# Performance work log

Hardware: AMD Instinct MI355X
Metric: run time of the kernel (lower is better)

## Reference

```python
import jax, jax.numpy as jnp
import numpy as np

NVFP4_VALUES = jnp.array([0.0, 0.5, 1.0, 1.5, 2.0, 3.0, 4.0, 6.0], dtype=jnp.float32)
NVFP4_MAX = 6.0


def quantize_to_nvfp4(t):
    """Fake-quantize to NVFP4 (e2m1) via nearest codebook magnitude.
    Returns (quantized_tensor, inv_scale) matching the torch reference."""
    amax = jnp.maximum(jnp.max(jnp.abs(t)), 1e-12)
    scale = NVFP4_MAX / amax                      # scalar
    scaled = jnp.clip(t.astype(jnp.float32) * scale, -NVFP4_MAX, NVFP4_MAX)
    signs = jnp.sign(scaled)
    # distance to each of the 8 e2m1 magnitudes -> nearest index
    dist = jnp.abs(jnp.abs(scaled)[..., None] - NVFP4_VALUES)  # (..., 8)
    idx = jnp.argmin(dist, axis=-1)
    quantized = signs * NVFP4_VALUES[idx]
    return quantized, 1.0 / scale


def setup_inputs() -> dict:
    key = jax.random.key(0)
    kx, kw = jax.random.split(key)
    x = jax.random.normal(kx, (512, 4096), dtype=jnp.float32)          # batch=512 (in SUPPORTED_BATCH_SIZES -> no padding)
    # kaiming-uniform-ish init for weight [out_features, in_features]
    bound = float(np.sqrt(6.0 / 4096.0))
    weight = jax.random.uniform(kw, (4096, 4096), dtype=jnp.float32,
                                minval=-bound, maxval=bound)
    return {"x": x, "weight": weight}


def reference(x, weight):
    # batch==512 is an exact supported size, so pad/unpad is identity.
    x_q, x_inv_scale = quantize_to_nvfp4(x)
    w_q, w_inv_scale = quantize_to_nvfp4(weight)
    # out[b,o] = sum_i (x_q*x_s)[b,i] * (w_q*w_s)[o,i]
    out = jnp.einsum('bi,oi->bo', x_q * x_inv_scale, w_q * w_inv_scale)
    return out.astype(x.dtype)
```

## Files before the change

### kernel.cpp

```cpp
#include <hip/hip_runtime.h>

#define M_DIM 512
#define N_DIM 4096
#define K_DIM 4096

typedef __attribute__((ext_vector_type(4))) float f32x4;
typedef __attribute__((ext_vector_type(8))) int i32x8;
typedef __attribute__((ext_vector_type(4))) int i32x4;

#define PART_X_OFF 0
#define PART_X_N   256
#define PART_W_OFF 256
#define PART_W_N   1024
#define AMAX_OFF   1280
#define XQ_BYTE_OFF 8192
#define WQ_BYTE_OFF (XQ_BYTE_OFF + M_DIM * K_DIM)

__global__ __launch_bounds__(256) void amax_kernel(
    const float4* __restrict__ x4, const float4* __restrict__ w4,
    float* __restrict__ ws_f) {
    const int b = blockIdx.x;
    float m = 0.0f;
    if (b < PART_X_N) {
        const int n4 = M_DIM * K_DIM / 4, stride = PART_X_N * 256;
        for (int i = b * 256 + threadIdx.x; i < n4; i += stride) {
            float4 a = x4[i];
            m = fmaxf(m, fmaxf(fmaxf(fabsf(a.x), fabsf(a.y)),
                               fmaxf(fabsf(a.z), fabsf(a.w))));
        }
    } else {
        const int n4 = N_DIM * K_DIM / 4, stride = PART_W_N * 256;
        for (int i = (b - PART_X_N) * 256 + threadIdx.x; i < n4; i += stride) {
            float4 a = w4[i];
            m = fmaxf(m, fmaxf(fmaxf(fabsf(a.x), fabsf(a.y)),
                               fmaxf(fabsf(a.z), fabsf(a.w))));
        }
    }
    for (int off = 32; off > 0; off >>= 1)
        m = fmaxf(m, __shfl_down(m, off, 64));
    __shared__ float sm[4];
    if ((threadIdx.x & 63) == 0) sm[threadIdx.x >> 6] = m;
    __syncthreads();
    if (threadIdx.x == 0) {
        m = fmaxf(fmaxf(sm[0], sm[1]), fmaxf(sm[2], sm[3]));
        ws_f[(b < PART_X_N) ? (PART_X_OFF + b) : (PART_W_OFF + b - PART_X_N)] = m;
    }
}

__device__ __forceinline__ unsigned int q1(float x, float s) {
    float a = fabsf(x) * s;
    unsigned int b;
    if      (a <= 0.25f) b = 0x00u;
    else if (a <= 0.75f) b = 0x30u;
    else if (a <= 1.25f) b = 0x38u;
    else if (a <= 1.75f) b = 0x3Cu;
    else if (a <= 2.5f)  b = 0x40u;
    else if (a <= 3.5f)  b = 0x44u;
    else if (a <= 5.0f)  b = 0x48u;
    else                 b = 0x4Cu;
    return b | ((__float_as_uint(x) >> 24) & 0x80u);
}
__device__ __forceinline__ unsigned int qpack4(float4 v, float s) {
    return q1(v.x, s) | (q1(v.y, s) << 8) | (q1(v.z, s) << 16) | (q1(v.w, s) << 24);
}

__global__ __launch_bounds__(256) void quant_kernel(
    const float4* __restrict__ x4, const float4* __restrict__ w4,
    float* __restrict__ ws_f, unsigned char* __restrict__ ws_b) {
    const int b = blockIdx.x, t = threadIdx.x;
    const bool is_x = b < 512;
    float m = 0.0f;
    if (is_x) {
        m = ws_f[PART_X_OFF + t];
    } else {
        for (int i = t; i < PART_W_N; i += 256)
            m = fmaxf(m, ws_f[PART_W_OFF + i]);
    }
    for (int off = 32; off > 0; off >>= 1)
        m = fmaxf(m, __shfl_down(m, off, 64));
    __shared__ float sm[4];
    if ((t & 63) == 0) sm[t >> 6] = m;
    __syncthreads();
    m = fmaxf(fmaxf(sm[0], sm[1]), fmaxf(sm[2], sm[3]));
    float amax = fmaxf(m, 1e-12f);
    float s = 6.0f / amax;
    if (t == 0 && b == 0)   ws_f[AMAX_OFF + 0] = amax;
    if (t == 0 && b == 512) ws_f[AMAX_OFF + 1] = amax;

    const float4* src = is_x ? x4 : w4;
    unsigned char* dstb = ws_b + (is_x ? XQ_BYTE_OFF : WQ_BYTE_OFF);
    const int idx16 = (is_x ? b : b - 512) * 256 + t;
    const float4* p = src + (size_t)idx16 * 4;
    uint4 o;
    o.x = qpack4(p[0], s);
    o.y = qpack4(p[1], s);
    o.z = qpack4(p[2], s);
    o.w = qpack4(p[3], s);
    ((uint4*)dstb)[idx16] = o;
}

__device__ __forceinline__ void async_copy16(const void* g, void* l) {
    __builtin_amdgcn_global_load_lds(
        (const __attribute__((address_space(1))) unsigned int*)g,
        (__attribute__((address_space(3))) unsigned int*)l, 16, 0, 0);
}

__device__ __forceinline__ i32x8 frag_load(const unsigned char* rowbase,
                                           int mask, int g0) {
    const i32x4 lo = *(const i32x4*)(rowbase + ((g0 ^ mask) * 16));
    const i32x4 hi = *(const i32x4*)(rowbase + (((g0 + 1) ^ mask) * 16));
    return __builtin_shufflevector(lo, hi, 0, 1, 2, 3, 4, 5, 6, 7);
}

__global__ __launch_bounds__(256, 2) void gemm_kernel(
    const unsigned char* __restrict__ A, const unsigned char* __restrict__ B,
    float* __restrict__ C, const float* __restrict__ amax2) {
    __shared__ __align__(16) unsigned char As[64 * 512];
    __shared__ __align__(16) unsigned char Bs[64 * 512];

    const int bid  = blockIdx.x;
    const int bm   = (bid >> 6) * 64;
    const int bn   = ((bid & 7) * 8 + ((bid >> 3) & 7)) * 64;
    const int tid  = threadIdx.x;
    const int lane = tid & 63;
    const int wave = tid >> 6;
    const int wm   = (wave >> 1) * 32;
    const int wn   = (wave & 1) * 32;
    const int t15  = lane & 15;
    const int quad = lane >> 4;

    const float cs = (1.0f / (6.0f / fmaxf(amax2[0], 1e-12f))) *
                     (1.0f / (6.0f / fmaxf(amax2[1], 1e-12f)));

    const unsigned char* agp[8];
    const unsigned char* bgp[8];
#pragma unroll
    for (int j = 0; j < 8; j++) {
        const int c = j * 256 + tid;
        const int row = c >> 5, pcol = c & 31;
        const int gk = pcol ^ (row & 31);
        agp[j] = A + (size_t)(bm + row) * K_DIM + gk * 16;
        bgp[j] = B + (size_t)(bn + row) * K_DIM + gk * 16;
    }

    f32x4 acc[2][2] = {};
    const unsigned char* A0 = As + (size_t)(wm + t15) * 512;
    const unsigned char* A1 = A0 + 16 * 512;
    const unsigned char* B0 = Bs + (size_t)(wn + t15) * 512;
    const unsigned char* B1 = B0 + 16 * 512;
    const int mk0 = t15, mk1 = t15 + 16;

    for (int ko = 0; ko < K_DIM; ko += 512) {
#pragma unroll
        for (int j = 0; j < 8; j++) {
            async_copy16(agp[j] + ko, As + (j * 256 + tid) * 16);
            async_copy16(bgp[j] + ko, Bs + (j * 256 + tid) * 16);
        }
        __syncthreads();

#pragma unroll
        for (int s = 0; s < 4; s++) {
            const int g0 = s * 8 + (quad << 1);
            const i32x8 af0 = frag_load(A0, mk0, g0);
            const i32x8 af1 = frag_load(A1, mk1, g0);
            const i32x8 bf0 = frag_load(B0, mk0, g0);
            const i32x8 bf1 = frag_load(B1, mk1, g0);
            acc[0][0] = __builtin_amdgcn_mfma_scale_f32_16x16x128_f8f6f4(
                af0, bf0, acc[0][0], 0, 0, 0, 0x7F7F7F7F, 0, 0x7F7F7F7F);
            acc[0][1] = __builtin_amdgcn_mfma_scale_f32_16x16x128_f8f6f4(
                af0, bf1, acc[0][1], 0, 0, 0, 0x7F7F7F7F, 0, 0x7F7F7F7F);
            acc[1][0] = __builtin_amdgcn_mfma_scale_f32_16x16x128_f8f6f4(
                af1, bf0, acc[1][0], 0, 0, 0, 0x7F7F7F7F, 0, 0x7F7F7F7F);
            acc[1][1] = __builtin_amdgcn_mfma_scale_f32_16x16x128_f8f6f4(
                af1, bf1, acc[1][1], 0, 0, 0, 0x7F7F7F7F, 0, 0x7F7F7F7F);
        }
        __syncthreads();
    }

#pragma unroll
    for (int i = 0; i < 2; i++)
#pragma unroll
        for (int j = 0; j < 2; j++) {
            const int m0 = bm + wm + i * 16 + quad * 4;
            const int n0 = bn + wn + j * 16 + t15;
#pragma unroll
            for (int r = 0; r < 4; r++)
                C[(size_t)(m0 + r) * N_DIM + n0] = acc[i][j][r] * cs;
        }
}

extern "C" void kernel_launch(void* const* d_in, const int* in_sizes, int n_in,
                              void* d_out, int out_size, void* d_ws, size_t ws_size,
                              hipStream_t stream) {
    const float* x = (const float*)d_in[0];
    const float* w = (const float*)d_in[1];
    float* out = (float*)d_out;

    float* ws_f = (float*)d_ws;
    unsigned char* ws_b = (unsigned char*)d_ws;
    const unsigned char* xq = ws_b + XQ_BYTE_OFF;
    const unsigned char* wq = ws_b + WQ_BYTE_OFF;

    amax_kernel<<<PART_X_N + PART_W_N, 256, 0, stream>>>(
        (const float4*)x, (const float4*)w, ws_f);
    quant_kernel<<<512 + 4096, 256, 0, stream>>>(
        (const float4*)x, (const float4*)w, ws_f, ws_b);
    gemm_kernel<<<(M_DIM / 64) * (N_DIM / 64), 256, 0, stream>>>(
        xq, wq, out, ws_f + AMAX_OFF);
}
```

Baseline: 134.4 us.

## Fuse amax, quantize and GEMM into one cooperative kernel with grid syncs

Replaces the three separate launches (amax reduction, quantization, GEMM) with one cooperative kernel of 512 blocks that uses grid.sync between phases. Each block computes partial amax for x and w, then after a grid barrier reduces the partials, quantizes its slice, and after another barrier runs the same MFMA GEMM tile. The aim is to remove launch overhead and inter-kernel gaps. The cost is that the memory-bound amax and quant phases now run on only 512 blocks with fixed unrolled loops, which may lower bandwidth utilisation, plus two grid-wide barriers. The old three-kernel path is kept as a fallback if the cooperative launch fails.

Result: slower. 263.4 us (+96.0%).

```diff
diff --git a/kernel.cpp b/kernel.cpp
--- a/kernel.cpp
+++ b/kernel.cpp
@@ -1,4 +1,7 @@
 #include <hip/hip_runtime.h>
+#include <hip/hip_cooperative_groups.h>
+
+namespace cg = cooperative_groups;
 
 #define M_DIM 512
 #define N_DIM 4096
@@ -8,6 +11,8 @@
 typedef __attribute__((ext_vector_type(8))) int i32x8;
 typedef __attribute__((ext_vector_type(4))) int i32x4;
 
+#define F_PART_X   0
+#define F_PART_W   512
 #define PART_X_OFF 0
 #define PART_X_N   256
 #define PART_W_OFF 256
@@ -15,37 +20,6 @@
 #define AMAX_OFF   1280
 #define XQ_BYTE_OFF 8192
 #define WQ_BYTE_OFF (XQ_BYTE_OFF + M_DIM * K_DIM)
-
-__global__ __launch_bounds__(256) void amax_kernel(
-    const float4* __restrict__ x4, const float4* __restrict__ w4,
-    float* __restrict__ ws_f) {
-    const int b = blockIdx.x;
-    float m = 0.0f;
-    if (b < PART_X_N) {
-        const int n4 = M_DIM * K_DIM / 4, stride = PART_X_N * 256;
-        for (int i = b * 256 + threadIdx.x; i < n4; i += stride) {
-            float4 a = x4[i];
-            m = fmaxf(m, fmaxf(fmaxf(fabsf(a.x), fabsf(a.y)),
-                               fmaxf(fabsf(a.z), fabsf(a.w))));
-        }
-    } else {
-        const int n4 = N_DIM * K_DIM / 4, stride = PART_W_N * 256;
-        for (int i = (b - PART_X_N) * 256 + threadIdx.x; i < n4; i += stride) {
-            float4 a = w4[i];
-            m = fmaxf(m, fmaxf(fmaxf(fabsf(a.x), fabsf(a.y)),
-                               fmaxf(fabsf(a.z), fabsf(a.w))));
-        }
-    }
-    for (int off = 32; off > 0; off >>= 1)
-        m = fmaxf(m, __shfl_down(m, off, 64));
-    __shared__ float sm[4];
-    if ((threadIdx.x & 63) == 0) sm[threadIdx.x >> 6] = m;
-    __syncthreads();
-    if (threadIdx.x == 0) {
-        m = fmaxf(fmaxf(sm[0], sm[1]), fmaxf(sm[2], sm[3]));
-        ws_f[(b < PART_X_N) ? (PART_X_OFF + b) : (PART_W_OFF + b - PART_X_N)] = m;
-    }
-}
 
 __device__ __forceinline__ unsigned int q1(float x, float s) {
     float a = fabsf(x) * s;
@@ -64,41 +38,6 @@
     return q1(v.x, s) | (q1(v.y, s) << 8) | (q1(v.z, s) << 16) | (q1(v.w, s) << 24);
 }
 
-__global__ __launch_bounds__(256) void quant_kernel(
-    const float4* __restrict__ x4, const float4* __restrict__ w4,
-    float* __restrict__ ws_f, unsigned char* __restrict__ ws_b) {
-    const int b = blockIdx.x, t = threadIdx.x;
-    const bool is_x = b < 512;
-    float m = 0.0f;
-    if (is_x) {
-        m = ws_f[PART_X_OFF + t];
-    } else {
-        for (int i = t; i < PART_W_N; i += 256)
-            m = fmaxf(m, ws_f[PART_W_OFF + i]);
-    }
-    for (int off = 32; off > 0; off >>= 1)
-        m = fmaxf(m, __shfl_down(m, off, 64));
-    __shared__ float sm[4];
-    if ((t & 63) == 0) sm[t >> 6] = m;
-    __syncthreads();
-    m = fmaxf(fmaxf(sm[0], sm[1]), fmaxf(sm[2], sm[3]));
-    float amax = fmaxf(m, 1e-12f);
-    float s = 6.0f / amax;
-    if (t == 0 && b == 0)   ws_f[AMAX_OFF + 0] = amax;
-    if (t == 0 && b == 512) ws_f[AMAX_OFF + 1] = amax;
-
-    const float4* src = is_x ? x4 : w4;
-    unsigned char* dstb = ws_b + (is_x ? XQ_BYTE_OFF : WQ_BYTE_OFF);
-    const int idx16 = (is_x ? b : b - 512) * 256 + t;
-    const float4* p = src + (size_t)idx16 * 4;
-    uint4 o;
-    o.x = qpack4(p[0], s);
-    o.y = qpack4(p[1], s);
-    o.z = qpack4(p[2], s);
-    o.w = qpack4(p[3], s);
-    ((uint4*)dstb)[idx16] = o;
-}
-
 __device__ __forceinline__ void async_copy16(const void* g, void* l) {
     __builtin_amdgcn_global_load_lds(
         (const __attribute__((address_space(1))) unsigned int*)g,
@@ -112,25 +51,93 @@
     return __builtin_shufflevector(lo, hi, 0, 1, 2, 3, 4, 5, 6, 7);
 }
 
-__global__ __launch_bounds__(256, 2) void gemm_kernel(
-    const unsigned char* __restrict__ A, const unsigned char* __restrict__ B,
-    float* __restrict__ C, const float* __restrict__ amax2) {
+__global__ __launch_bounds__(256, 2) void fused_kernel(
+    const float4* __restrict__ x4, const float4* __restrict__ w4,
+    float* __restrict__ C, float* __restrict__ ws_f,
+    unsigned char* __restrict__ ws_b) {
     __shared__ __align__(16) unsigned char As[64 * 512];
     __shared__ __align__(16) unsigned char Bs[64 * 512];
 
-    const int bid  = blockIdx.x;
-    const int bm   = (bid >> 6) * 64;
-    const int bn   = ((bid & 7) * 8 + ((bid >> 3) & 7)) * 64;
-    const int tid  = threadIdx.x;
+    const int b = blockIdx.x;
+    const int tid = threadIdx.x;
+    cg::grid_group grid = cg::this_grid();
+    float* sred = (float*)As;
+
+    {
+        float mx = 0.0f, mw = 0.0f;
+        const int base = b * 256 + tid, stride = 512 * 256;
+#pragma unroll
+        for (int j = 0; j < 4; j++) {
+            float4 a = x4[base + j * stride];
+            mx = fmaxf(mx, fmaxf(fmaxf(fabsf(a.x), fabsf(a.y)),
+                                 fmaxf(fabsf(a.z), fabsf(a.w))));
+        }
+#pragma unroll
+        for (int j = 0; j < 32; j++) {
+            float4 a = w4[base + j * stride];
+            mw = fmaxf(mw, fmaxf(fmaxf(fabsf(a.x), fabsf(a.y)),
+                                 fmaxf(fabsf(a.z), fabsf(a.w))));
+        }
+        for (int off = 32; off > 0; off >>= 1) {
+            mx = fmaxf(mx, __shfl_down(mx, off, 64));
+            mw = fmaxf(mw, __shfl_down(mw, off, 64));
+        }
+        if ((tid & 63) == 0) { sred[tid >> 6] = mx; sred[4 + (tid >> 6)] = mw; }
+        __syncthreads();
+        if (tid == 0) {
+            ws_f[F_PART_X + b] = fmaxf(fmaxf(sred[0], sred[1]),
+                                       fmaxf(sred[2], sred[3]));
+            ws_f[F_PART_W + b] = fmaxf(fmaxf(sred[4], sred[5]),
+                                       fmaxf(sred[6], sred[7]));
+        }
+    }
+    grid.sync();
+
+    float ax, aw;
+    {
+        float mx = fmaxf(ws_f[F_PART_X + tid], ws_f[F_PART_X + 256 + tid]);
+        float mw = fmaxf(ws_f[F_PART_W + tid], ws_f[F_PART_W + 256 + tid]);
+        for (int off = 32; off > 0; off >>= 1) {
+            mx = fmaxf(mx, __shfl_down(mx, off, 64));
+            mw = fmaxf(mw, __shfl_down(mw, off, 64));
+        }
+        if ((tid & 63) == 0) { sred[tid >> 6] = mx; sred[4 + (tid >> 6)] = mw; }
+        __syncthreads();
+        ax = fmaxf(fmaxf(fmaxf(sred[0], sred[1]), fmaxf(sred[2], sred[3])), 1e-12f);
+        aw = fmaxf(fmaxf(fmaxf(sred[4], sred[5]), fmaxf(sred[6], sred[7])), 1e-12f);
+        const float sx = 6.0f / ax, sw = 6.0f / aw;
+
+        {
+            const int idx16 = b * 256 + tid;
+            const float4* p = x4 + (size_t)idx16 * 4;
+            uint4 o;
+            o.x = qpack4(p[0], sx); o.y = qpack4(p[1], sx);
+            o.z = qpack4(p[2], sx); o.w = qpack4(p[3], sx);
+            ((uint4*)(ws_b + XQ_BYTE_OFF))[idx16] = o;
+        }
+#pragma unroll
+        for (int j = 0; j < 8; j++) {
+            const int idx16 = b * 2048 + j * 256 + tid;
+            const float4* p = w4 + (size_t)idx16 * 4;
+            uint4 o;
+            o.x = qpack4(p[0], sw); o.y = qpack4(p[1], sw);
+            o.z = qpack4(p[2], sw); o.w = qpack4(p[3], sw);
+            ((uint4*)(ws_b + WQ_BYTE_OFF))[idx16] = o;
+        }
+    }
+    const float cs = (1.0f / (6.0f / ax)) * (1.0f / (6.0f / aw));
+    grid.sync();
+
+    const unsigned char* A = ws_b + XQ_BYTE_OFF;
+    const unsigned char* B = ws_b + WQ_BYTE_OFF;
+    const int bm   = (b >> 6) * 64;
+    const int bn   = ((b & 7) * 8 + ((b >> 3) & 7)) * 64;
     const int lane = tid & 63;
     const int wave = tid >> 6;
     const int wm   = (wave >> 1) * 32;
     const int wn   = (wave & 1) * 32;
     const int t15  = lane & 15;
     const int quad = lane >> 4;
-
-    const float cs = (1.0f / (6.0f / fmaxf(amax2[0], 1e-12f))) *
-                     (1.0f / (6.0f / fmaxf(amax2[1], 1e-12f)));
 
     const unsigned char* agp[8];
     const unsigned char* bgp[8];
@@ -189,22 +196,166 @@
         }
 }
 
+__global__ __launch_bounds__(256) void amax_kernel(
+    const float4* __restrict__ x4, const float4* __restrict__ w4,
+    float* __restrict__ ws_f) {
+    const int b = blockIdx.x;
+    float m = 0.0f;
+    if (b < PART_X_N) {
+        const int n4 = M_DIM * K_DIM / 4, stride = PART_X_N * 256;
+        for (int i = b * 256 + threadIdx.x; i < n4; i += stride) {
+            float4 a = x4[i];
+            m = fmaxf(m, fmaxf(fmaxf(fabsf(a.x), fabsf(a.y)),
+                               fmaxf(fabsf(a.z), fabsf(a.w))));
+        }
+    } else {
+        const int n4 = N_DIM * K_DIM / 4, stride = PART_W_N * 256;
+        for (int i = (b - PART_X_N) * 256 + threadIdx.x; i < n4; i += stride) {
+            float4 a = w4[i];
+            m = fmaxf(m, fmaxf(fmaxf(fabsf(a.x), fabsf(a.y)),
+                               fmaxf(fabsf(a.z), fabsf(a.w))));
+        }
+    }
+    for (int off = 32; off > 0; off >>= 1)
+        m = fmaxf(m, __shfl_down(m, off, 64));
+    __shared__ float sm[4];
+    if ((threadIdx.x & 63) == 0) sm[threadIdx.x >> 6] = m;
+    __syncthreads();
+    if (threadIdx.x == 0) {
+        m = fmaxf(fmaxf(sm[0], sm[1]), fmaxf(sm[2], sm[3]));
+        ws_f[(b < PART_X_N) ? (PART_X_OFF + b) : (PART_W_OFF + b - PART_X_N)] = m;
+    }
+}
+
+__global__ __launch_bounds__(256) void quant_kernel(
+    const float4* __restrict__ x4, const float4* __restrict__ w4,
+    float* __restrict__ ws_f, unsigned char* __restrict__ ws_b) {
+    const int b = blockIdx.x, t = threadIdx.x;
+    const bool is_x = b < 512;
+    float m = 0.0f;
+    if (is_x) {
+        m = ws_f[PART_X_OFF + t];
+    } else {
+        for (int i = t; i < PART_W_N; i += 256)
+            m = fmaxf(m, ws_f[PART_W_OFF + i]);
+    }
+    for (int off = 32; off > 0; off >>= 1)
+        m = fmaxf(m, __shfl_down(m, off, 64));
+    __shared__ float sm[4];
+    if ((t & 63) == 0) sm[t >> 6] = m;
+    __syncthreads();
+    m = fmaxf(fmaxf(sm[0], sm[1]), fmaxf(sm[2], sm[3]));
+    float amax = fmaxf(m, 1e-12f);
+    float s = 6.0f / amax;
+    if (t == 0 && b == 0)   ws_f[AMAX_OFF + 0] = amax;
+    if (t == 0 && b == 512) ws_f[AMAX_OFF + 1] = amax;
+
+    const float4* src = is_x ? x4 : w4;
+    unsigned char* dstb = ws_b + (is_x ? XQ_BYTE_OFF : WQ_BYTE_OFF);
+    const int idx16 = (is_x ? b : b - 512) * 256 + t;
+    const float4* p = src + (size_t)idx16 * 4;
+    uint4 o;
+    o.x = qpack4(p[0], s); o.y = qpack4(p[1], s);
+    o.z = qpack4(p[2], s); o.w = qpack4(p[3], s);
+    ((uint4*)dstb)[idx16] = o;
+}
+
+__global__ __launch_bounds__(256, 2) void gemm_kernel(
+    const unsigned char* __restrict__ A, const unsigned char* __restrict__ B,
+    float* __restrict__ C, const float* __restrict__ amax2) {
+    __shared__ __align__(16) unsigned char As[64 * 512];
+    __shared__ __align__(16) unsigned char Bs[64 * 512];
+
+    const int bid  = blockIdx.x;
+    const int bm   = (bid >> 6) * 64;
+    const int bn   = ((bid & 7) * 8 + ((bid >> 3) & 7)) * 64;
+    const int tid  = threadIdx.x;
+    const int lane = tid & 63;
+    const int wave = tid >> 6;
+    const int wm   = (wave >> 1) * 32;
+    const int wn   = (wave & 1) * 32;
+    const int t15  = lane & 15;
+    const int quad = lane >> 4;
+
+    const float cs = (1.0f / (6.0f / fmaxf(amax2[0], 1e-12f))) *
+                     (1.0f / (6.0f / fmaxf(amax2[1], 1e-12f)));
+
+    const unsigned char* agp[8];
+    const unsigned char* bgp[8];
+#pragma unroll
+    for (int j = 0; j < 8; j++) {
+        const int c = j * 256 + tid;
+        const int row = c >> 5, pcol = c & 31;
+        const int gk = pcol ^ (row & 31);
+        agp[j] = A + (size_t)(bm + row) * K_DIM + gk * 16;
+        bgp[j] = B + (size_t)(bn + row) * K_DIM + gk * 16;
+    }
+
+    f32x4 acc[2][2] = {};
+    const unsigned char* A0 = As + (size_t)(wm + t15) * 512;
+    const unsigned char* A1 = A0 + 16 * 512;
+    const unsigned char* B0 = Bs + (size_t)(wn + t15) * 512;
+    const unsigned char* B1 = B0 + 16 * 512;
+    const int mk0 = t15, mk1 = t15 + 16;
+
+    for (int ko = 0; ko < K_DIM; ko += 512) {
+#pragma unroll
+        for (int j = 0; j < 8; j++) {
+            async_copy16(agp[j] + ko, As + (j * 256 + tid) * 16);
+            async_copy16(bgp[j] + ko, Bs + (j * 256 + tid) * 16);
+        }
+        __syncthreads();
+
+#pragma unroll
+        for (int s = 0; s < 4; s++) {
+            const int g0 = s * 8 + (quad << 1);
+            const i32x8 af0 = frag_load(A0, mk0, g0);
+            const i32x8 af1 = frag_load(A1, mk1, g0);
+            const i32x8 bf0 = frag_load(B0, mk0, g0);
+            const i32x8 bf1 = frag_load(B1, mk1, g0);
+            acc[0][0] = __builtin_amdgcn_mfma_scale_f32_16x16x128_f8f6f4(
+                af0, bf0, acc[0][0], 0, 0, 0, 0x7F7F7F7F, 0, 0x7F7F7F7F);
+            acc[0][1] = __builtin_amdgcn_mfma_scale_f32_16x16x128_f8f6f4(
+                af0, bf1, acc[0][1], 0, 0, 0, 0x7F7F7F7F, 0, 0x7F7F7F7F);
+            acc[1][0] = __builtin_amdgcn_mfma_scale_f32_16x16x128_f8f6f4(
+                af1, bf0, acc[1][0], 0, 0, 0, 0x7F7F7F7F, 0, 0x7F7F7F7F);
+            acc[1][1] = __builtin_amdgcn_mfma_scale_f32_16x16x128_f8f6f4(
+                af1, bf1, acc[1][1], 0, 0, 0, 0x7F7F7F7F, 0, 0x7F7F7F7F);
+        }
+        __syncthreads();
+    }
+
+#pragma unroll
+    for (int i = 0; i < 2; i++)
+#pragma unroll
+        for (int j = 0; j < 2; j++) {
+            const int m0 = bm + wm + i * 16 + quad * 4;
+            const int n0 = bn + wn + j * 16 + t15;
+#pragma unroll
+            for (int r = 0; r < 4; r++)
+                C[(size_t)(m0 + r) * N_DIM + n0] = acc[i][j][r] * cs;
+        }
+}
+
 extern "C" void kernel_launch(void* const* d_in, const int* in_sizes, int n_in,
                               void* d_out, int out_size, void* d_ws, size_t ws_size,
                               hipStream_t stream) {
-    const float* x = (const float*)d_in[0];
-    const float* w = (const float*)d_in[1];
+    const float4* x4 = (const float4*)d_in[0];
+    const float4* w4 = (const float4*)d_in[1];
     float* out = (float*)d_out;
-
     float* ws_f = (float*)d_ws;
     unsigned char* ws_b = (unsigned char*)d_ws;
-    const unsigned char* xq = ws_b + XQ_BYTE_OFF;
-    const unsigned char* wq = ws_b + WQ_BYTE_OFF;
-
-    amax_kernel<<<PART_X_N + PART_W_N, 256, 0, stream>>>(
-        (const float4*)x, (const float4*)w, ws_f);
-    quant_kernel<<<512 + 4096, 256, 0, stream>>>(
-        (const float4*)x, (const float4*)w, ws_f, ws_b);
-    gemm_kernel<<<(M_DIM / 64) * (N_DIM / 64), 256, 0, stream>>>(
-        xq, wq, out, ws_f + AMAX_OFF);
-}
+
+    void* args[5] = {(void*)&x4, (void*)&w4, (void*)&out, (void*)&ws_f,
+                     (void*)&ws_b};
+    hipError_t err = hipLaunchCooperativeKernel(
+        (const void*)fused_kernel, dim3(512), dim3(256), args, 0, stream);
+    if (err != hipSuccess) {
+        const unsigned char* xq = ws_b + XQ_BYTE_OFF;
+        const unsigned char* wq = ws_b + WQ_BYTE_OFF;
+        amax_kernel<<<PART_X_N + PART_W_N, 256, 0, stream>>>(x4, w4, ws_f);
+        quant_kernel<<<512 + 4096, 256, 0, stream>>>(x4, w4, ws_f, ws_b);
+        gemm_kernel<<<(M_DIM / 64) * (N_DIM / 64), 256, 0, stream>>>(
+            xq, wq, out, ws_f + AMAX_OFF);
+    }
+}
```
